# Kernel optimization log

Hardware: AMD Instinct MI355X
Metric: run time of the kernel (lower is better)

Reference implementation:

```python
import jax, jax.numpy as jnp
import numpy as np

B, T, I, H, O = 128, 1024, 256, 1024, 256


def setup_inputs() -> dict:
    key = jax.random.key(0)
    k = jax.random.split(key, 6)
    inp = jax.random.normal(k[0], (B, T, I), dtype=jnp.float32)
    hPrevious = jnp.zeros((1, B, H), dtype=jnp.float32)
    # IRNN init: W_hh = I, biases = 0, W_ih ~ N(0,1)/H
    W_ih = jax.random.normal(k[1], (H, I), dtype=jnp.float32) / H
    W_hh = jnp.eye(H, dtype=jnp.float32)
    b_ih = jnp.zeros((H,), dtype=jnp.float32)
    b_hh = jnp.zeros((H,), dtype=jnp.float32)
    bound = 1.0 / np.sqrt(H)
    W_out = jax.random.uniform(k[2], (O, H), dtype=jnp.float32, minval=-bound, maxval=bound)
    b_out = jax.random.uniform(k[3], (O,), dtype=jnp.float32, minval=-bound, maxval=bound)
    return {"inp": inp, "hPrevious": hPrevious, "W_ih": W_ih, "W_hh": W_hh,
            "b_ih": b_ih, "b_hh": b_hh, "W_out": W_out, "b_out": b_out}


def reference(inp, hPrevious, W_ih, W_hh, b_ih, b_hh, W_out, b_out):
    # Precompute input projections for all timesteps: [T, B, H]
    x_proj = jnp.einsum('bti,hi->tbh', inp, W_ih) + (b_ih + b_hh)

    def step(h, xp):
        h_new = jax.nn.relu(xp + h @ W_hh.T)  # [B, H]
        return h_new, None

    h0 = hPrevious[0]  # [B, H]
    h_final, _ = jax.lax.scan(step, h0, x_proj)
    out = h_final @ W_out.T + b_out  # [B, O]
    return out
```

## Files before the change

### kernel.cpp

```cpp
#include <hip/hip_runtime.h>
#include <hip/hip_bf16.h>
#include <stdint.h>

#define B_ 128
#define T_ 1024
#define I_ 256
#define H_ 1024
#define O_ 256
#define NJ 128
#define TM 128
#define SA 72
#define SX 132

typedef __attribute__((ext_vector_type(8))) short short8;
typedef __attribute__((ext_vector_type(4))) short s16x4;
typedef __attribute__((ext_vector_type(4))) float f32x4;

__device__ __forceinline__ unsigned short f2bf(float x) {
  __hip_bfloat16 h = __float2bfloat16(x);
  unsigned short u;
  __builtin_memcpy(&u, &h, 2);
  return u;
}
__device__ __forceinline__ float bf2f(short s) {
  return __uint_as_float(((unsigned)(unsigned short)s) << 16);
}

__global__ void k_prep(const float* __restrict__ b_ih, const float* __restrict__ b_hh,
                       float* __restrict__ bias, const float4* __restrict__ Wih,
                       ushort4* __restrict__ Wb, const float* __restrict__ Whh,
                       int* flag, const float4* __restrict__ inp,
                       ushort4* __restrict__ Abf) {
  int gid = blockIdx.x * 256 + threadIdx.x;
  if (gid < H_) bias[gid] = b_ih[gid] + b_hh[gid];
  if (gid < H_ * I_ / 4) {
    float4 f = Wih[gid];
    ushort4 u;
    u.x = f2bf(f.x); u.y = f2bf(f.y); u.z = f2bf(f.z); u.w = f2bf(f.w);
    Wb[gid] = u;
  }
  if (gid < (H_ * H_) / 4) {
    bool bad = false;
    #pragma unroll
    for (int q = 0; q < 4; ++q) {
      int e = gid * 4 + q;
      int r = e >> 10, c = e & (H_ - 1);
      float expect = (r == c) ? 1.0f : 0.0f;
      if (Whh[e] != expect) bad = true;
    }
    if (bad) atomicOr(flag, 1);
  }
  const int NV = B_ * T_ * I_ / 4;
  for (int v = gid; v < NV; v += 524288) {
    float4 f = inp[v];
    ushort4 u;
    u.x = f2bf(f.x); u.y = f2bf(f.y); u.z = f2bf(f.z); u.w = f2bf(f.w);
    Abf[v] = u;
  }
}

__global__ __launch_bounds__(256, 2) void k_main(
    const __hip_bfloat16* __restrict__ Abf, const __hip_bfloat16* __restrict__ Wb,
    const float* __restrict__ bias, const float* __restrict__ hPrev,
    float* __restrict__ hOut, const int* __restrict__ flag,
    const float* __restrict__ inp, const float* __restrict__ W_ih,
    const float* __restrict__ W_hh) {
  __shared__ __align__(16) __hip_bfloat16 As[2][TM * SA];
  __shared__ __align__(16) __hip_bfloat16 Xs[NJ * SX];
  __shared__ float sComb[256];
  const int bx = blockIdx.x, tid = threadIdx.x;

  if (*flag != 0) {
    if (bx >= B_) return;
    float* h1 = (float*)Xs;
    float* h2 = h1 + H_;
    float* xr = h2 + H_;
    int b = bx;
    for (int j = tid; j < H_; j += 256) h1[j] = hPrev[b * H_ + j];
    __syncthreads();
    for (int t = 0; t < T_; ++t) {
      for (int k = tid; k < I_; k += 256) xr[k] = inp[((size_t)b * T_ + t) * I_ + k];
      __syncthreads();
      for (int j = tid; j < H_; j += 256) {
        float s = bias[j];
        for (int k = 0; k < I_; ++k) s += W_ih[(size_t)j * I_ + k] * xr[k];
        for (int k = 0; k < H_; ++k) s += W_hh[(size_t)j * H_ + k] * h1[k];
        h2[j] = fmaxf(s, 0.f);
      }
      __syncthreads();
      for (int j = tid; j < H_; j += 256) h1[j] = h2[j];
      __syncthreads();
    }
    for (int j = tid; j < H_; j += 256) hOut[b * H_ + j] = h1[j];
    return;
  }

  const int xcd = bx & 7, loc = bx >> 3;
  const int b  = xcd * 16 + (loc >> 3);
  const int n0 = (loc & 7) * NJ;

  const int w = tid >> 6, l = tid & 63;
  const int wm = (w >> 1) * 64, wn = (w & 1) * 64;
  const int lr = l & 15, lg = l >> 4;
  const int rA = tid >> 1;
  const int cAe = (tid & 1) * 32;
  const int jlane = tid & 127;

  const __hip_bfloat16* Ab = Abf + (size_t)b * T_ * I_;

  short8 bfr[4][8];
  #pragma unroll
  for (int ni = 0; ni < 4; ++ni)
    #pragma unroll
    for (int ks = 0; ks < 8; ++ks)
      bfr[ni][ks] = *(const short8*)(Wb + (size_t)(n0 + wn + ni * 16 + lr) * I_ + ks * 32 + lg * 8);

  float bj = bias[n0 + jlane];
  float hrun = (tid < NJ) ? hPrev[b * H_ + n0 + tid] : 0.f;

  f32x4 acc[4][4];
  #pragma unroll
  for (int i = 0; i < 4; ++i)
    #pragma unroll
    for (int j = 0; j < 4; ++j) acc[i][j] = (f32x4){0.f, 0.f, 0.f, 0.f};

  short8 rb0, rb1, rb2, rb3;
#define LOADRB(s) { const __hip_bfloat16* _a = Ab + ((size_t)(((s) >> 2) * TM + rA)) * I_ + ((s) & 3) * 64 + cAe; \
    rb0 = *(const short8*)(_a); rb1 = *(const short8*)(_a + 8); \
    rb2 = *(const short8*)(_a + 16); rb3 = *(const short8*)(_a + 24); }
#define STAGERB(buf) { __hip_bfloat16* _d = &As[buf][rA * SA + cAe]; \
    *(short8*)(_d) = rb0; *(short8*)(_d + 8) = rb1; \
    *(short8*)(_d + 16) = rb2; *(short8*)(_d + 24) = rb3; }

  LOADRB(0); STAGERB(0); LOADRB(1);
  __syncthreads();

  int cur = 0;
  for (int ig = 0; ig < 8; ++ig) {
    #pragma unroll
    for (int k = 0; k < 4; ++k) {
      const int s = ig * 4 + k;
      #pragma unroll
      for (int kk = 0; kk < 2; ++kk) {
        short8 af[4];
        #pragma unroll
        for (int mi = 0; mi < 4; ++mi)
          af[mi] = *(const short8*)&As[cur][(wm + mi * 16 + lr) * SA + kk * 32 + lg * 8];
        #pragma unroll
        for (int mi = 0; mi < 4; ++mi)
          #pragma unroll
          for (int ni = 0; ni < 4; ++ni)
            acc[mi][ni] = __builtin_amdgcn_mfma_f32_16x16x32_bf16(
                af[mi], bfr[ni][k * 2 + kk], acc[mi][ni], 0, 0, 0);
      }
      if (s < 31) STAGERB(cur ^ 1);
      if (s < 30) LOADRB(s + 2);
      if (k == 3) {
        #pragma unroll
        for (int mi = 0; mi < 4; ++mi)
          #pragma unroll
          for (int ni = 0; ni < 4; ++ni) {
            s16x4 pv;
            #pragma unroll
            for (int r = 0; r < 4; ++r) pv[r] = (short)f2bf(acc[mi][ni][r]);
            *(s16x4*)&Xs[(wn + ni * 16 + lr) * SX + wm + mi * 16 + lg * 4] = pv;
            acc[mi][ni] = (f32x4){0.f, 0.f, 0.f, 0.f};
          }
      }
      __syncthreads();
      cur ^= 1;
    }
    if (tid < NJ) {
      float hr = hrun;
      #pragma unroll
      for (int c = 0; c < 16; ++c) {
        s16x4 v = *(const s16x4*)&Xs[tid * SX + c * 4];
        #pragma unroll
        for (int r = 0; r < 4; ++r) hr = fmaxf(bf2f(v[r]) + bj + hr, 0.f);
      }
      hrun = hr;
    } else {
      float Asg = 0.f, Csg = 0.f;
      #pragma unroll
      for (int c = 0; c < 16; ++c) {
        s16x4 v = *(const s16x4*)&Xs[jlane * SX + 64 + c * 4];
        #pragma unroll
        for (int r = 0; r < 4; ++r) {
          float x = bf2f(v[r]) + bj;
          Asg += x;
          Csg = fmaxf(Csg + x, 0.f);
        }
      }
      sComb[2 * jlane] = Asg;
      sComb[2 * jlane + 1] = Csg;
    }
    __syncthreads();
    if (tid < NJ) hrun = fmaxf(sComb[2 * tid + 1], sComb[2 * tid] + hrun);
  }
  if (tid < NJ) hOut[b * H_ + n0 + tid] = hrun;
#undef LOADRB
#undef STAGERB
}

__global__ __launch_bounds__(256) void k_out(const float* __restrict__ h,
                                             const float* __restrict__ Wo,
                                             const float* __restrict__ bo,
                                             float* __restrict__ out) {
  __shared__ float hs[H_];
  int b = blockIdx.x, o = threadIdx.x;
  #pragma unroll
  for (int q = 0; q < 4; ++q) hs[o + q * 256] = h[b * H_ + o + q * 256];
  __syncthreads();
  const float4* wrow = (const float4*)(Wo + (size_t)o * H_);
  float s = bo[o];
  #pragma unroll 4
  for (int j4 = 0; j4 < H_ / 4; ++j4) {
    float4 wv = wrow[j4];
    s += hs[j4 * 4] * wv.x + hs[j4 * 4 + 1] * wv.y + hs[j4 * 4 + 2] * wv.z + hs[j4 * 4 + 3] * wv.w;
  }
  out[b * O_ + o] = s;
}

extern "C" void kernel_launch(void* const* d_in, const int* in_sizes, int n_in,
                              void* d_out, int out_size, void* d_ws, size_t ws_size,
                              hipStream_t stream) {
  const float* inp   = (const float*)d_in[0];
  const float* hPrev = (const float*)d_in[1];
  const float* W_ih  = (const float*)d_in[2];
  const float* W_hh  = (const float*)d_in[3];
  const float* b_ih  = (const float*)d_in[4];
  const float* b_hh  = (const float*)d_in[5];
  const float* W_out = (const float*)d_in[6];
  const float* b_out = (const float*)d_in[7];
  float* out = (float*)d_out;

  char* ws = (char*)d_ws;
  int*   flag = (int*)ws;
  float* bias = (float*)(ws + 1024);
  float* h    = (float*)(ws + 8192);
  __hip_bfloat16* Wb  = (__hip_bfloat16*)(ws + (1u << 20));
  __hip_bfloat16* Abf = (__hip_bfloat16*)(ws + (2u << 20));

  hipMemsetAsync(flag, 0, 4, stream);
  k_prep<<<2048, 256, 0, stream>>>(b_ih, b_hh, bias, (const float4*)W_ih,
                                   (ushort4*)Wb, W_hh, flag,
                                   (const float4*)inp, (ushort4*)Abf);
  k_main<<<1024, 256, 0, stream>>>(Abf, Wb, bias, hPrev, h, flag, inp, W_ih, W_hh);
  k_out<<<128, 256, 0, stream>>>(h, W_out, b_out, out);
}
```

Baseline: 147.8 us.

## Compose ReLU recurrence segments in registers via wave shuffles instead of LDS scan

The per-timestep ReLU recurrence is written as an affine max-plus map f(h)=max(C, A+h). Each MFMA accumulator tile is now folded into (A,C) pairs directly in registers, and lanes are combined with xor shuffles across the 16-lane groups. This replaces the bf16 staging of projections into shared memory and the 64-step serial scan run by half the threads, and drops one barrier per 128-timestep group. It also keeps projections in fp32 instead of rounding them to bf16, at the cost of extra shuffles and ALU work in the epilogue.

```diff
diff --git a/kernel.cpp b/kernel.cpp
--- a/kernel.cpp
+++ b/kernel.cpp
@@ -10,10 +10,8 @@
 #define NJ 128
 #define TM 128
 #define SA 72
-#define SX 132
 
 typedef __attribute__((ext_vector_type(8))) short short8;
-typedef __attribute__((ext_vector_type(4))) short s16x4;
 typedef __attribute__((ext_vector_type(4))) float f32x4;
 
 __device__ __forceinline__ unsigned short f2bf(float x) {
@@ -21,9 +19,6 @@
   unsigned short u;
   __builtin_memcpy(&u, &h, 2);
   return u;
-}
-__device__ __forceinline__ float bf2f(short s) {
-  return __uint_as_float(((unsigned)(unsigned short)s) << 16);
 }
 
 __global__ void k_prep(const float* __restrict__ b_ih, const float* __restrict__ b_hh,
@@ -65,14 +60,13 @@
     float* __restrict__ hOut, const int* __restrict__ flag,
     const float* __restrict__ inp, const float* __restrict__ W_ih,
     const float* __restrict__ W_hh) {
-  __shared__ __align__(16) __hip_bfloat16 As[2][TM * SA];
-  __shared__ __align__(16) __hip_bfloat16 Xs[NJ * SX];
-  __shared__ float sComb[256];
+  __shared__ __align__(16) __hip_bfloat16 AsT[2][TM * SA];
+  __shared__ float2 sPair[2][NJ];
   const int bx = blockIdx.x, tid = threadIdx.x;
 
   if (*flag != 0) {
     if (bx >= B_) return;
-    float* h1 = (float*)Xs;
+    float* h1 = (float*)AsT;
     float* h2 = h1 + H_;
     float* xr = h2 + H_;
     int b = bx;
@@ -104,7 +98,6 @@
   const int lr = l & 15, lg = l >> 4;
   const int rA = tid >> 1;
   const int cAe = (tid & 1) * 32;
-  const int jlane = tid & 127;
 
   const __hip_bfloat16* Ab = Abf + (size_t)b * T_ * I_;
 
@@ -115,7 +108,10 @@
     for (int ks = 0; ks < 8; ++ks)
       bfr[ni][ks] = *(const short8*)(Wb + (size_t)(n0 + wn + ni * 16 + lr) * I_ + ks * 32 + lg * 8);
 
-  float bj = bias[n0 + jlane];
+  float bj4[4];
+  #pragma unroll
+  for (int ni = 0; ni < 4; ++ni) bj4[ni] = bias[n0 + wn + ni * 16 + lr];
+
   float hrun = (tid < NJ) ? hPrev[b * H_ + n0 + tid] : 0.f;
 
   f32x4 acc[4][4];
@@ -128,7 +124,7 @@
 #define LOADRB(s) { const __hip_bfloat16* _a = Ab + ((size_t)(((s) >> 2) * TM + rA)) * I_ + ((s) & 3) * 64 + cAe; \
     rb0 = *(const short8*)(_a); rb1 = *(const short8*)(_a + 8); \
     rb2 = *(const short8*)(_a + 16); rb3 = *(const short8*)(_a + 24); }
-#define STAGERB(buf) { __hip_bfloat16* _d = &As[buf][rA * SA + cAe]; \
+#define STAGERB(buf) { __hip_bfloat16* _d = &AsT[buf][rA * SA + cAe]; \
     *(short8*)(_d) = rb0; *(short8*)(_d + 8) = rb1; \
     *(short8*)(_d + 16) = rb2; *(short8*)(_d + 24) = rb3; }
 
@@ -145,7 +141,7 @@
         short8 af[4];
         #pragma unroll
         for (int mi = 0; mi < 4; ++mi)
-          af[mi] = *(const short8*)&As[cur][(wm + mi * 16 + lr) * SA + kk * 32 + lg * 8];
+          af[mi] = *(const short8*)&AsT[cur][(wm + mi * 16 + lr) * SA + kk * 32 + lg * 8];
         #pragma unroll
         for (int mi = 0; mi < 4; ++mi)
           #pragma unroll
@@ -156,46 +152,50 @@
       if (s < 31) STAGERB(cur ^ 1);
       if (s < 30) LOADRB(s + 2);
       if (k == 3) {
+        const int wmIdx = w >> 1;
         #pragma unroll
-        for (int mi = 0; mi < 4; ++mi)
+        for (int ni = 0; ni < 4; ++ni) {
+          float bj = bj4[ni];
+          float Acomp = 0.f, Ccomp = 0.f;
           #pragma unroll
-          for (int ni = 0; ni < 4; ++ni) {
-            s16x4 pv;
-            #pragma unroll
-            for (int r = 0; r < 4; ++r) pv[r] = (short)f2bf(acc[mi][ni][r]);
-            *(s16x4*)&Xs[(wn + ni * 16 + lr) * SX + wm + mi * 16 + lg * 4] = pv;
+          for (int mi = 0; mi < 4; ++mi) {
+            float x0 = acc[mi][ni][0] + bj;
+            float x1 = acc[mi][ni][1] + bj;
+            float x2 = acc[mi][ni][2] + bj;
+            float x3 = acc[mi][ni][3] + bj;
+            float Aseg = ((x0 + x1) + x2) + x3;
+            float Cseg = fmaxf(fmaxf(x1, 0.f) + x2, 0.f);
+            Cseg = fmaxf(Cseg + x3, 0.f);
+            float Ap = __shfl_xor(Aseg, 16);
+            float Cp = __shfl_xor(Cseg, 16);
+            {
+              bool late = (l & 16) != 0;
+              float Al = late ? Aseg : Ap, Cl = late ? Cseg : Cp, Ce = late ? Cp : Cseg;
+              Aseg += Ap;
+              Cseg = fmaxf(Cl, Al + Ce);
+            }
+            Ap = __shfl_xor(Aseg, 32);
+            Cp = __shfl_xor(Cseg, 32);
+            {
+              bool late = (l & 32) != 0;
+              float Al = late ? Aseg : Ap, Cl = late ? Cseg : Cp, Ce = late ? Cp : Cseg;
+              Aseg += Ap;
+              Cseg = fmaxf(Cl, Al + Ce);
+            }
+            if (mi == 0) { Acomp = Aseg; Ccomp = Cseg; }
+            else { Ccomp = fmaxf(Cseg, Aseg + Ccomp); Acomp += Aseg; }
             acc[mi][ni] = (f32x4){0.f, 0.f, 0.f, 0.f};
           }
-      }
-      __syncthreads();
-      cur ^= 1;
-    }
-    if (tid < NJ) {
-      float hr = hrun;
-      #pragma unroll
-      for (int c = 0; c < 16; ++c) {
-        s16x4 v = *(const s16x4*)&Xs[tid * SX + c * 4];
-        #pragma unroll
-        for (int r = 0; r < 4; ++r) hr = fmaxf(bf2f(v[r]) + bj + hr, 0.f);
-      }
-      hrun = hr;
-    } else {
-      float Asg = 0.f, Csg = 0.f;
-      #pragma unroll
-      for (int c = 0; c < 16; ++c) {
-        s16x4 v = *(const s16x4*)&Xs[jlane * SX + 64 + c * 4];
-        #pragma unroll
-        for (int r = 0; r < 4; ++r) {
-          float x = bf2f(v[r]) + bj;
-          Asg += x;
-          Csg = fmaxf(Csg + x, 0.f);
+          if (lg == 0) sPair[wmIdx][wn + ni * 16 + lr] = make_float2(Acomp, Ccomp);
         }
       }
-      sComb[2 * jlane] = Asg;
-      sComb[2 * jlane + 1] = Csg;
-    }
-    __syncthreads();
-    if (tid < NJ) hrun = fmaxf(sComb[2 * tid + 1], sComb[2 * tid] + hrun);
+      __syncthreads();
+      cur ^= 1;
+    }
+    if (tid < NJ) {
+      float2 p0 = sPair[0][tid], p1 = sPair[1][tid];
+      hrun = fmaxf(p1.y, p1.x + fmaxf(p0.y, p0.x + hrun));
+    }
   }
   if (tid < NJ) hOut[b * H_ + n0 + tid] = hrun;
 #undef LOADRB
```

Measured after the change: 161.4 us. 1.09x slower.
